# Kernel tuning notes

Hardware: AMD Instinct MI355X
Metric: run time of the kernel (lower is better)

## Reference

```python
import jax, jax.numpy as jnp
import numpy as np

NS, NV = 48, 10            # scalar / vector multiplicities
IN_SIZE = NS + 3*NV + 3*NV + NS   # 156
N_EDGE_FEAT = 96
HIDDEN = 96
# weight shapes per output irrep: 0e:(58,48) 1o:(68,10) 1e:(68,10) 0o:(58,48)
W_SHAPES = [('0e', NS + NV, NS), ('1o', NS + 2*NV, NV), ('1e', 2*NV + NS, NV), ('0o', NV + NS, NS)]
WEIGHT_NUMEL = sum(a*b for _, a, b in W_SHAPES)  # 6928
N_NODES, N_EDGES = 10000, 50000


def setup_inputs() -> dict:
    key = jax.random.key(0)
    ks = jax.random.split(key, 9)
    node_attr = jax.random.normal(ks[0], (N_NODES, IN_SIZE), dtype=jnp.float32)
    edge_index = jax.random.randint(ks[1], (2, N_EDGES), 0, N_NODES)
    edge_attr = jax.random.normal(ks[2], (N_EDGES, N_EDGE_FEAT), dtype=jnp.float32)
    edge_sh = jax.random.normal(ks[3], (N_EDGES, 4), dtype=jnp.float32)
    s1 = 1.0 / np.sqrt(N_EDGE_FEAT)
    s2 = 1.0 / np.sqrt(HIDDEN)
    W1 = jax.random.normal(ks[4], (N_EDGE_FEAT, HIDDEN), dtype=jnp.float32) * s1
    b1 = jnp.zeros((HIDDEN,), dtype=jnp.float32)
    W2 = jax.random.normal(ks[5], (HIDDEN, WEIGHT_NUMEL), dtype=jnp.float32) * s2
    b2 = jnp.zeros((WEIGHT_NUMEL,), dtype=jnp.float32)
    return {'node_attr': node_attr, 'edge_index': edge_index, 'edge_attr': edge_attr,
            'edge_sh': edge_sh, 'W1': W1, 'b1': b1, 'W2': W2, 'b2': b2}


def _faster_tp(in_, sh, weight):
    # in_: [E, 156], sh: [E, 4], weight: [E, 6928]
    in_0e = in_[:, :NS]                                   # [E,48]
    in_1o = in_[:, NS:NS + 3*NV].reshape(-1, NV, 3)       # [E,10,3]
    in_1e = in_[:, NS + 3*NV:NS + 6*NV].reshape(-1, NV, 3)
    in_0o = in_[:, NS + 6*NV:]                            # [E,48]
    sh_0e = sh[:, 0]                                      # [E]
    sh_1o = sh[:, 1:]                                     # [E,3]
    inv_s3 = 1.0 / np.sqrt(3.0)
    inv_s2 = 1.0 / np.sqrt(2.0)

    out_0e = jnp.concatenate([
        in_0e * sh_0e[:, None],
        jnp.sum(in_1o * sh_1o[:, None, :], axis=-1) * inv_s3], axis=-1)      # [E,58]
    out_1o = jnp.concatenate([
        in_0e[:, :, None] * sh_1o[:, None, :],
        in_1o * sh_0e[:, None, None],
        jnp.cross(in_1e, sh_1o[:, None, :]) * inv_s2], axis=-2)              # [E,68,3]
    out_1e = jnp.concatenate([
        jnp.cross(in_1o, sh_1o[:, None, :]) * inv_s2,
        in_1e * sh_0e[:, None, None],
        in_0o[:, :, None] * sh_1o[:, None, :]], axis=-2)                     # [E,68,3]
    out_0o = jnp.concatenate([
        jnp.sum(in_1e * sh_1o[:, None, :], axis=-1) * inv_s3,
        in_0o * sh_0e[:, None]], axis=-1)                                    # [E,58]

    wd = {}
    start = 0
    for name, a, b in W_SHAPES:
        wd[name] = weight[:, start:start + a*b].reshape(-1, a, b) / np.sqrt(a)
        start += a*b

    o0e = jnp.einsum('ei,eio->eo', out_0e, wd['0e'])                 # [E,48]
    o1o = jnp.einsum('eic,eio->eoc', out_1o, wd['1o']).reshape(-1, 3*NV)
    o1e = jnp.einsum('eic,eio->eoc', out_1e, wd['1e']).reshape(-1, 3*NV)
    o0o = jnp.einsum('ei,eio->eo', out_0o, wd['0o'])                 # [E,48]
    return jnp.concatenate([o0e, o1o, o1e, o0o], axis=-1)           # [E,156]


def reference(node_attr, edge_index, edge_attr, edge_sh, W1, b1, W2, b2):
    edge_src, edge_dst = edge_index[0], edge_index[1]
    # edge MLP -> per-edge TP weights
    h = jax.nn.relu(edge_attr @ W1 + b1)
    w = h @ W2 + b2                                       # [E, 6928]
    tp = _faster_tp(node_attr[edge_dst], edge_sh, w)      # [E, 156]
    # scatter-mean over source nodes
    n = node_attr.shape[0]
    seg = jax.ops.segment_sum(tp, edge_src, num_segments=n)
    cnt = jax.ops.segment_sum(jnp.ones((tp.shape[0],), tp.dtype), edge_src, num_segments=n)
    out = seg / jnp.maximum(cnt, 1.0)[:, None]
    # residual (in/out sizes equal, so pad is a no-op)
    return out + node_attr
```

## Files before the change

### kernel.cpp

```cpp
#include <hip/hip_runtime.h>

#define NE 50000
#define NN 10000
#define KH 96
#define WN 6928
#define NTILE 484
#define IN_SZ 156
#define EPW 32

typedef __attribute__((ext_vector_type(8))) short short8;
typedef __attribute__((ext_vector_type(4))) float float4v;

__device__ __forceinline__ unsigned short f2bf(float x) {
  unsigned u = __float_as_uint(x);
  unsigned r = (u + 0x7FFFu + ((u >> 16) & 1u)) >> 16;
  return (unsigned short)r;
}
__device__ __forceinline__ float b2f(unsigned short u) {
  return __uint_as_float(((unsigned)u) << 16);
}

__device__ __forceinline__ void issue3(short8 (&B)[3], float &bv,
                                       const unsigned short* p, const float* pb) {
  asm volatile("global_load_dwordx4 %0, %4, off\n\t"
               "global_load_dwordx4 %1, %4, off offset:1024\n\t"
               "global_load_dwordx4 %2, %4, off offset:2048\n\t"
               "global_load_dword %3, %5, off"
               : "=&v"(B[0]), "=&v"(B[1]), "=&v"(B[2]), "=&v"(bv)
               : "v"(p), "v"(pb));
}
__device__ __forceinline__ void waitB8(short8 (&B)[3], float &bv) {
  asm volatile("s_waitcnt vmcnt(8)"
               : "+v"(B[0]), "+v"(B[1]), "+v"(B[2]), "+v"(bv));
}
__device__ __forceinline__ void waitB4(short8 (&B)[3], float &bv) {
  asm volatile("s_waitcnt vmcnt(4)"
               : "+v"(B[0]), "+v"(B[1]), "+v"(B[2]), "+v"(bv));
}
__device__ __forceinline__ void waitB0(short8 (&B)[3], float &bv) {
  asm volatile("s_waitcnt vmcnt(0)"
               : "+v"(B[0]), "+v"(B[1]), "+v"(B[2]), "+v"(bv));
}

__device__ __forceinline__ int col_of_np(int np) {
  if (np < 2784) return np;
  if (np < 3872) { int rel = np - 2784, i = rel >> 4, o = rel & 15; return (o < 10) ? 2784 + i * 10 + o : -1; }
  if (np < 4960) { int rel = np - 3872, i = rel >> 4, o = rel & 15; return (o < 10) ? 3464 + i * 10 + o : -1; }
  return 4144 + (np - 4960);
}

__global__ __launch_bounds__(256) void w1t_kernel(
    const float* __restrict__ W1, unsigned short* __restrict__ W1T)
{
  int j = blockIdx.x * 256 + threadIdx.x;
  if (j < KH * KH) {
    int c = j / KH, k = j - c * KH;
    W1T[c * KH + k] = f2bf(W1[k * KH + c]);
  }
}

__global__ __launch_bounds__(384) void mlp1_kernel(
    const float* __restrict__ edge_attr, const unsigned short* __restrict__ W1T,
    const float* __restrict__ b1, unsigned short* __restrict__ h_ext)
{
  const int tid = threadIdx.x;
  const int e0 = blockIdx.x * 16;
  const int w = tid >> 6, l = tid & 15, q = (tid >> 4) & 3;

  short8 a[3], b[3];
  #pragma unroll
  for (int s = 0; s < 3; ++s) {
    const float* pa = edge_attr + (size_t)(e0 + l) * KH + s * 32 + q * 8;
    float4 x = *(const float4*)pa, y = *(const float4*)(pa + 4);
    short8 t;
    t[0] = (short)f2bf(x.x); t[1] = (short)f2bf(x.y);
    t[2] = (short)f2bf(x.z); t[3] = (short)f2bf(x.w);
    t[4] = (short)f2bf(y.x); t[5] = (short)f2bf(y.y);
    t[6] = (short)f2bf(y.z); t[7] = (short)f2bf(y.w);
    a[s] = t;
    b[s] = *(const short8*)(W1T + (size_t)(w * 16 + l) * KH + s * 32 + q * 8);
  }
  float4v C = {0.f, 0.f, 0.f, 0.f};
  #pragma unroll
  for (int s = 0; s < 3; ++s)
    C = __builtin_amdgcn_mfma_f32_16x16x32_bf16(a[s], b[s], C, 0, 0, 0);

  float bv = b1[w * 16 + l];
  #pragma unroll
  for (int r = 0; r < 4; ++r)
    h_ext[(size_t)(e0 + q * 4 + r) * KH + w * 16 + l] = f2bf(fmaxf(C[r] + bv, 0.f));
}

__global__ __launch_bounds__(256) void w2pt_kernel(
    const float* __restrict__ W2, const float* __restrict__ b2,
    unsigned short* __restrict__ W2PT, float* __restrict__ b2PT)
{
  int gid = blockIdx.x * 256 + threadIdx.x;
  if (gid < NTILE * 192) {
    int lane = gid & 63, s = (gid >> 6) % 3, t = gid / 192;
    int l = lane & 15, q = lane >> 4;
    int c = col_of_np(t * 16 + l);
    int kbase = s * 32 + q * 8;
    unsigned short o8[8];
    #pragma unroll
    for (int j = 0; j < 8; ++j) {
      int k = kbase + j;
      float v = (c >= 0) ? W2[(size_t)k * WN + c] : 0.f;
      o8[j] = f2bf(v);
    }
    uint4 pk;
    pk.x = o8[0] | ((unsigned)o8[1] << 16);
    pk.y = o8[2] | ((unsigned)o8[3] << 16);
    pk.z = o8[4] | ((unsigned)o8[5] << 16);
    pk.w = o8[6] | ((unsigned)o8[7] << 16);
    *(uint4*)(W2PT + (size_t)gid * 8) = pk;
  } else {
    int j = gid - NTILE * 192;
    if (j < NTILE * 16) {
      int c = col_of_np(j);
      b2PT[j] = (c >= 0) ? b2[c] : 0.f;
    }
  }
}

__global__ __launch_bounds__(512, 4) void tp_kernel(
    const unsigned short* __restrict__ h_ext, const float* __restrict__ node_attr,
    const int* __restrict__ edge_index, const float* __restrict__ edge_sh,
    const unsigned short* __restrict__ W2PT, const float* __restrict__ b2PT,
    float* __restrict__ acc, int* __restrict__ icnt)
{
  __shared__ unsigned short sIn[EPW][160];
  __shared__ float sOut[EPW][IN_SZ];
  __shared__ unsigned short sF0[2][60][EPW];
  __shared__ unsigned short sF1[2][68][3][EPW];
  __shared__ float sShs[EPW][4];
  __shared__ int sSrc[EPW], sDst[EPW];

  const int tid = threadIdx.x;
  const int e0 = blockIdx.x * EPW;

  if (tid < EPW) {
    int ok = (e0 + tid) < NE;
    int s = ok ? edge_index[e0 + tid] : 0;
    int d = ok ? edge_index[NE + e0 + tid] : 0;
    sSrc[tid] = s; sDst[tid] = d;
    if (ok) atomicAdd(&icnt[s], 1);
  }
  if (tid >= 128 && tid < 256) {
    int t2 = tid - 128;
    int e = t2 >> 2, c = t2 & 3;
    sShs[e][c] = ((e0 + e) < NE) ? edge_sh[(size_t)(e0 + e) * 4 + c] : 0.f;
  }
  __syncthreads();

  for (int idx = tid; idx < EPW * IN_SZ; idx += 512) {
    int e = idx / IN_SZ, f = idx - e * IN_SZ;
    sIn[e][f] = f2bf(node_attr[(size_t)sDst[e] * IN_SZ + f]);
  }
  for (int idx = tid; idx < EPW * IN_SZ; idx += 512) (&sOut[0][0])[idx] = 0.f;
  __syncthreads();

  {
    const int e = tid >> 4, j = tid & 15;
    const float sh0 = sShs[e][0], sx = sShs[e][1], sy = sShs[e][2], sz = sShs[e][3];
    const float i3 = 0.57735026918962576f, i2 = 0.70710678118654752f;
    for (int i = j; i < 48; i += 16) {
      float v0 = b2f(sIn[e][i]), w0 = b2f(sIn[e][108 + i]);
      sF0[0][i][e] = f2bf(v0 * sh0);
      sF0[1][10 + i][e] = f2bf(w0 * sh0);
      sF1[0][i][0][e] = f2bf(v0 * sx); sF1[0][i][1][e] = f2bf(v0 * sy); sF1[0][i][2][e] = f2bf(v0 * sz);
      sF1[1][20 + i][0][e] = f2bf(w0 * sx); sF1[1][20 + i][1][e] = f2bf(w0 * sy); sF1[1][20 + i][2][e] = f2bf(w0 * sz);
    }
    if (j < 10) {
      const int v = j;
      float ax = b2f(sIn[e][48 + 3 * v]), ay = b2f(sIn[e][48 + 3 * v + 1]), az = b2f(sIn[e][48 + 3 * v + 2]);
      float bx = b2f(sIn[e][78 + 3 * v]), by = b2f(sIn[e][78 + 3 * v + 1]), bz = b2f(sIn[e][78 + 3 * v + 2]);
      sF0[0][48 + v][e] = f2bf((ax * sx + ay * sy + az * sz) * i3);
      sF0[1][v][e]      = f2bf((bx * sx + by * sy + bz * sz) * i3);
      sF1[0][48 + v][0][e] = f2bf(ax * sh0); sF1[0][48 + v][1][e] = f2bf(ay * sh0); sF1[0][48 + v][2][e] = f2bf(az * sh0);
      sF1[0][58 + v][0][e] = f2bf((by * sz - bz * sy) * i2);
      sF1[0][58 + v][1][e] = f2bf((bz * sx - bx * sz) * i2);
      sF1[0][58 + v][2][e] = f2bf((bx * sy - by * sx) * i2);
      sF1[1][v][0][e] = f2bf((ay * sz - az * sy) * i2);
      sF1[1][v][1][e] = f2bf((az * sx - ax * sz) * i2);
      sF1[1][v][2][e] = f2bf((ax * sy - ay * sx) * i2);
      sF1[1][10 + v][0][e] = f2bf(bx * sh0); sF1[1][10 + v][1][e] = f2bf(by * sh0); sF1[1][10 + v][2][e] = f2bf(bz * sh0);
    }
  }
  if (tid < 128) {
    int fam = tid >> 6, i = 58 + ((tid >> 5) & 1), e = tid & 31;
    sF0[fam][i][e] = 0;
  }
  __syncthreads();

  const int wv = tid >> 6, l = tid & 15, q = (tid >> 4) & 3;

  short8 Af[2][3];
  #pragma unroll
  for (int m = 0; m < 2; ++m) {
    const unsigned short* ar = h_ext + (size_t)(e0 + m * 16 + l) * KH + q * 8;
    #pragma unroll
    for (int s = 0; s < 3; ++s) Af[m][s] = *(const short8*)(ar + s * 32);
  }

  const unsigned short* wlane = W2PT + (size_t)(tid & 63) * 8;
  const float* blane = b2PT + l;

  if (wv < 4) {
    const int sf = wv >> 1;
    const int ibeg = (wv & 1) * 30;
    const int tb = sf ? 310 : 0;
    const int obase = sf ? 108 : 0;
    #pragma unroll 1
    for (int ob = 0; ob < 3; ++ob) {
      float a0[4] = {0.f, 0.f, 0.f, 0.f}, a1[4] = {0.f, 0.f, 0.f, 0.f};
      short8 Ba[3], Bb[3], Bc[3];
      float vA, vB, vC;
      auto taddr = [&](int ii) -> size_t {
        int i = ibeg + ii; if (i >= 58) i = ibeg;
        return (size_t)(tb + 3 * i + ob);
      };
      auto body = [&](const short8 (&B)[3], float bv, int ii) {
        int i = ibeg + ii;
        ushort4 f0 = *(const ushort4*)&sF0[sf][i][q * 4];
        ushort4 f1 = *(const ushort4*)&sF0[sf][i][16 + q * 4];
        float4v C0 = {bv, bv, bv, bv}, C1 = {bv, bv, bv, bv};
        #pragma unroll
        for (int s = 0; s < 3; ++s) {
          C0 = __builtin_amdgcn_mfma_f32_16x16x32_bf16(Af[0][s], B[s], C0, 0, 0, 0);
          C1 = __builtin_amdgcn_mfma_f32_16x16x32_bf16(Af[1][s], B[s], C1, 0, 0, 0);
        }
        a0[0] += C0[0] * b2f(f0.x); a0[1] += C0[1] * b2f(f0.y);
        a0[2] += C0[2] * b2f(f0.z); a0[3] += C0[3] * b2f(f0.w);
        a1[0] += C1[0] * b2f(f1.x); a1[1] += C1[1] * b2f(f1.y);
        a1[2] += C1[2] * b2f(f1.z); a1[3] += C1[3] * b2f(f1.w);
      };
      { size_t t = taddr(0); issue3(Ba, vA, wlane + t * 1536, blane + t * 16); }
      { size_t t = taddr(1); issue3(Bb, vB, wlane + t * 1536, blane + t * 16); }
      { size_t t = taddr(2); issue3(Bc, vC, wlane + t * 1536, blane + t * 16); }
      #pragma unroll 1
      for (int ii = 0; ii < 27; ii += 3) {
        waitB8(Ba, vA); body(Ba, vA, ii);
        { size_t t = taddr(ii + 3); issue3(Ba, vA, wlane + t * 1536, blane + t * 16); }
        waitB8(Bb, vB); body(Bb, vB, ii + 1);
        { size_t t = taddr(ii + 4); issue3(Bb, vB, wlane + t * 1536, blane + t * 16); }
        waitB8(Bc, vC); body(Bc, vC, ii + 2);
        { size_t t = taddr(ii + 5); issue3(Bc, vC, wlane + t * 1536, blane + t * 16); }
      }
      waitB8(Ba, vA); body(Ba, vA, 27);
      waitB4(Bb, vB); body(Bb, vB, 28);
      waitB0(Bc, vC); body(Bc, vC, 29);
      const int col = obase + ob * 16 + l;
      #pragma unroll
      for (int r = 0; r < 4; ++r) {
        unsafeAtomicAdd(&sOut[q * 4 + r][col], a0[r]);
        unsafeAtomicAdd(&sOut[16 + q * 4 + r][col], a1[r]);
      }
    }
  } else {
    const int vf = (wv >> 1) - 2;
    const int ibeg = (wv & 1) * 34;
    const int tb = vf ? 242 : 174;
    float r0[4][3] = {{0.f}}, r1[4][3] = {{0.f}};
    short8 Ba[3], Bb[3];
    float vA, vB;
    auto tadr = [&](int ii) -> size_t { return (size_t)(tb + ibeg + ii); };
    auto body = [&](const short8 (&B)[3], float bv, int ii) {
      int i = ibeg + ii;
      ushort4 g0[3], g1[3];
      #pragma unroll
      for (int cc = 0; cc < 3; ++cc) {
        g0[cc] = *(const ushort4*)&sF1[vf][i][cc][q * 4];
        g1[cc] = *(const ushort4*)&sF1[vf][i][cc][16 + q * 4];
      }
      float4v C0 = {bv, bv, bv, bv}, C1 = {bv, bv, bv, bv};
      #pragma unroll
      for (int s = 0; s < 3; ++s) {
        C0 = __builtin_amdgcn_mfma_f32_16x16x32_bf16(Af[0][s], B[s], C0, 0, 0, 0);
        C1 = __builtin_amdgcn_mfma_f32_16x16x32_bf16(Af[1][s], B[s], C1, 0, 0, 0);
      }
      #pragma unroll
      for (int cc = 0; cc < 3; ++cc) {
        r0[0][cc] += C0[0] * b2f(g0[cc].x); r0[1][cc] += C0[1] * b2f(g0[cc].y);
        r0[2][cc] += C0[2] * b2f(g0[cc].z); r0[3][cc] += C0[3] * b2f(g0[cc].w);
        r1[0][cc] += C1[0] * b2f(g1[cc].x); r1[1][cc] += C1[1] * b2f(g1[cc].y);
        r1[2][cc] += C1[2] * b2f(g1[cc].z); r1[3][cc] += C1[3] * b2f(g1[cc].w);
      }
    };
    { size_t t = tadr(0); issue3(Ba, vA, wlane + t * 1536, blane + t * 16); }
    { size_t t = tadr(1); issue3(Bb, vB, wlane + t * 1536, blane + t * 16); }
    #pragma unroll 1
    for (int ii = 0; ii < 32; ii += 2) {
      waitB4(Ba, vA); body(Ba, vA, ii);
      { size_t t = tadr(ii + 2); issue3(Ba, vA, wlane + t * 1536, blane + t * 16); }
      waitB4(Bb, vB); body(Bb, vB, ii + 1);
      { size_t t = tadr(ii + 3); issue3(Bb, vB, wlane + t * 1536, blane + t * 16); }
    }
    waitB4(Ba, vA); body(Ba, vA, 32);
    waitB0(Bb, vB); body(Bb, vB, 33);
    if (l < 10) {
      const int col = (vf ? 78 : 48) + 3 * l;
      #pragma unroll
      for (int r = 0; r < 4; ++r)
        #pragma unroll
        for (int cc = 0; cc < 3; ++cc) {
          unsafeAtomicAdd(&sOut[q * 4 + r][col + cc], r0[r][cc]);
          unsafeAtomicAdd(&sOut[16 + q * 4 + r][col + cc], r1[r][cc]);
        }
    }
  }
  __syncthreads();

  const float n58 = 0.13130643285972254f, n68 = 0.12126781251816650f;
  for (int idx = tid; idx < EPW * IN_SZ; idx += 512) {
    int e = idx / IN_SZ, o = idx - e * IN_SZ;
    if (e0 + e < NE) {
      float nrm = (o < 48 || o >= 108) ? n58 : n68;
      unsafeAtomicAdd(&acc[(size_t)sSrc[e] * IN_SZ + o], sOut[e][o] * nrm);
    }
  }
}

__global__ __launch_bounds__(256) void finalize_kernel(
    const float* __restrict__ acc, const int* __restrict__ icnt,
    const float* __restrict__ node_attr, float* __restrict__ out)
{
  int idx = blockIdx.x * 256 + threadIdx.x;
  if (idx < NN * IN_SZ) {
    int n = idx / IN_SZ;
    out[idx] = acc[idx] / fmaxf((float)icnt[n], 1.f) + node_attr[idx];
  }
}

extern "C" void kernel_launch(void* const* d_in, const int* in_sizes, int n_in,
                              void* d_out, int out_size, void* d_ws, size_t ws_size,
                              hipStream_t stream)
{
  const float* node_attr  = (const float*)d_in[0];
  const int*   edge_index = (const int*)d_in[1];
  const float* edge_attr  = (const float*)d_in[2];
  const float* edge_sh    = (const float*)d_in[3];
  const float* W1 = (const float*)d_in[4];
  const float* b1 = (const float*)d_in[5];
  const float* W2 = (const float*)d_in[6];
  const float* b2 = (const float*)d_in[7];
  float* out = (float*)d_out;

  unsigned short* h_ext = (unsigned short*)d_ws;
  unsigned short* W2PT  = h_ext + (size_t)50016 * KH;
  float* b2PT = (float*)(W2PT + (size_t)NTILE * 1536);
  float* acc  = b2PT + (size_t)NTILE * 16;
  int*   icnt = (int*)(acc + (size_t)NN * IN_SZ);
  unsigned short* W1T = (unsigned short*)(icnt + NN);

  w1t_kernel<<<(KH * KH + 255) / 256, 256, 0, stream>>>(W1, W1T);
  w2pt_kernel<<<(NTILE * 208 + 255) / 256, 256, 0, stream>>>(W2, b2, W2PT, b2PT);
  mlp1_kernel<<<NE / 16, 384, 0, stream>>>(edge_attr, W1T, b1, h_ext);
  hipMemsetAsync(acc, 0, (size_t)NN * IN_SZ * sizeof(float), stream);
  hipMemsetAsync(icnt, 0, (size_t)NN * sizeof(int), stream);
  hipMemsetAsync(h_ext + (size_t)NE * KH, 0, (size_t)16 * KH * sizeof(unsigned short), stream);
  tp_kernel<<<(NE + EPW - 1) / EPW, 512, 0, stream>>>(h_ext, node_attr, edge_index,
                                                      edge_sh, W2PT, b2PT, acc, icnt);
  finalize_kernel<<<(NN * IN_SZ + 255) / 256, 256, 0, stream>>>(acc, icnt, node_attr, out);
}
```

Measured before the change: 312.3 us.

## Merge prep kernels and memsets, read node_attr directly, rebalance scalar work across waves

Folds the W1 transpose, the W2 pack and the three memsets into one prep kernel, cutting launch and memset overhead. In the TP kernel, the bf16 staging of gathered node_attr in shared memory is dropped; features are built straight from global loads, which removes a barrier and shared-memory traffic. The scalar-irrep input rows are split so the vector waves also take 8 rows each, evening out work across the 8 waves. The shrunken sF0 and uneven padding paths add some risk, and the direct global reads are uncoalesced per lane.

```diff
diff --git a/kernel.cpp b/kernel.cpp
--- a/kernel.cpp
+++ b/kernel.cpp
@@ -10,6 +10,8 @@
 
 typedef __attribute__((ext_vector_type(8))) short short8;
 typedef __attribute__((ext_vector_type(4))) float float4v;
+
+template<int N> struct IC { static constexpr int n = N; };
 
 __device__ __forceinline__ unsigned short f2bf(float x) {
   unsigned u = __float_as_uint(x);
@@ -49,13 +51,56 @@
   return 4144 + (np - 4960);
 }
 
-__global__ __launch_bounds__(256) void w1t_kernel(
-    const float* __restrict__ W1, unsigned short* __restrict__ W1T)
-{
-  int j = blockIdx.x * 256 + threadIdx.x;
-  if (j < KH * KH) {
+#define R0 (NTILE * 192)
+#define R1 (R0 + NTILE * 16)
+#define R2 (R1 + KH * KH)
+#define R3 (R2 + NN * IN_SZ / 4)
+#define R4 (R3 + NN / 4)
+#define R5 (R4 + 192)
+__global__ __launch_bounds__(256) void prep_kernel(
+    const float* __restrict__ W2, const float* __restrict__ b2,
+    const float* __restrict__ W1,
+    unsigned short* __restrict__ W2PT, float* __restrict__ b2PT,
+    unsigned short* __restrict__ W1T,
+    float* __restrict__ acc, int* __restrict__ icnt,
+    unsigned short* __restrict__ h_ext)
+{
+  int gid = blockIdx.x * 256 + threadIdx.x;
+  if (gid < R0) {
+    int lane = gid & 63, s = (gid >> 6) % 3, t = gid / 192;
+    int l = lane & 15, q = lane >> 4;
+    int c = col_of_np(t * 16 + l);
+    int kbase = s * 32 + q * 8;
+    unsigned short o8[8];
+    #pragma unroll
+    for (int j = 0; j < 8; ++j) {
+      int k = kbase + j;
+      float v = (c >= 0) ? W2[(size_t)k * WN + c] : 0.f;
+      o8[j] = f2bf(v);
+    }
+    uint4 pk;
+    pk.x = o8[0] | ((unsigned)o8[1] << 16);
+    pk.y = o8[2] | ((unsigned)o8[3] << 16);
+    pk.z = o8[4] | ((unsigned)o8[5] << 16);
+    pk.w = o8[6] | ((unsigned)o8[7] << 16);
+    *(uint4*)(W2PT + (size_t)gid * 8) = pk;
+  } else if (gid < R1) {
+    int j = gid - R0;
+    int c = col_of_np(j);
+    b2PT[j] = (c >= 0) ? b2[c] : 0.f;
+  } else if (gid < R2) {
+    int j = gid - R1;
     int c = j / KH, k = j - c * KH;
     W1T[c * KH + k] = f2bf(W1[k * KH + c]);
+  } else if (gid < R3) {
+    uint4 z = {0, 0, 0, 0};
+    ((uint4*)acc)[gid - R2] = z;
+  } else if (gid < R4) {
+    uint4 z = {0, 0, 0, 0};
+    ((uint4*)icnt)[gid - R3] = z;
+  } else if (gid < R5) {
+    uint4 z = {0, 0, 0, 0};
+    ((uint4*)(h_ext + (size_t)NE * KH))[gid - R4] = z;
   }
 }
 
@@ -91,47 +136,14 @@
     h_ext[(size_t)(e0 + q * 4 + r) * KH + w * 16 + l] = f2bf(fmaxf(C[r] + bv, 0.f));
 }
 
-__global__ __launch_bounds__(256) void w2pt_kernel(
-    const float* __restrict__ W2, const float* __restrict__ b2,
-    unsigned short* __restrict__ W2PT, float* __restrict__ b2PT)
-{
-  int gid = blockIdx.x * 256 + threadIdx.x;
-  if (gid < NTILE * 192) {
-    int lane = gid & 63, s = (gid >> 6) % 3, t = gid / 192;
-    int l = lane & 15, q = lane >> 4;
-    int c = col_of_np(t * 16 + l);
-    int kbase = s * 32 + q * 8;
-    unsigned short o8[8];
-    #pragma unroll
-    for (int j = 0; j < 8; ++j) {
-      int k = kbase + j;
-      float v = (c >= 0) ? W2[(size_t)k * WN + c] : 0.f;
-      o8[j] = f2bf(v);
-    }
-    uint4 pk;
-    pk.x = o8[0] | ((unsigned)o8[1] << 16);
-    pk.y = o8[2] | ((unsigned)o8[3] << 16);
-    pk.z = o8[4] | ((unsigned)o8[5] << 16);
-    pk.w = o8[6] | ((unsigned)o8[7] << 16);
-    *(uint4*)(W2PT + (size_t)gid * 8) = pk;
-  } else {
-    int j = gid - NTILE * 192;
-    if (j < NTILE * 16) {
-      int c = col_of_np(j);
-      b2PT[j] = (c >= 0) ? b2[c] : 0.f;
-    }
-  }
-}
-
 __global__ __launch_bounds__(512, 4) void tp_kernel(
     const unsigned short* __restrict__ h_ext, const float* __restrict__ node_attr,
     const int* __restrict__ edge_index, const float* __restrict__ edge_sh,
     const unsigned short* __restrict__ W2PT, const float* __restrict__ b2PT,
     float* __restrict__ acc, int* __restrict__ icnt)
 {
-  __shared__ unsigned short sIn[EPW][160];
   __shared__ float sOut[EPW][IN_SZ];
-  __shared__ unsigned short sF0[2][60][EPW];
+  __shared__ unsigned short sF0[2][58][EPW];
   __shared__ unsigned short sF1[2][68][3][EPW];
   __shared__ float sShs[EPW][4];
   __shared__ int sSrc[EPW], sDst[EPW];
@@ -153,19 +165,13 @@
   }
   __syncthreads();
 
-  for (int idx = tid; idx < EPW * IN_SZ; idx += 512) {
-    int e = idx / IN_SZ, f = idx - e * IN_SZ;
-    sIn[e][f] = f2bf(node_attr[(size_t)sDst[e] * IN_SZ + f]);
-  }
-  for (int idx = tid; idx < EPW * IN_SZ; idx += 512) (&sOut[0][0])[idx] = 0.f;
-  __syncthreads();
-
   {
     const int e = tid >> 4, j = tid & 15;
+    const float* na = node_attr + (size_t)sDst[e] * IN_SZ;
     const float sh0 = sShs[e][0], sx = sShs[e][1], sy = sShs[e][2], sz = sShs[e][3];
     const float i3 = 0.57735026918962576f, i2 = 0.70710678118654752f;
     for (int i = j; i < 48; i += 16) {
-      float v0 = b2f(sIn[e][i]), w0 = b2f(sIn[e][108 + i]);
+      float v0 = na[i], w0 = na[108 + i];
       sF0[0][i][e] = f2bf(v0 * sh0);
       sF0[1][10 + i][e] = f2bf(w0 * sh0);
       sF1[0][i][0][e] = f2bf(v0 * sx); sF1[0][i][1][e] = f2bf(v0 * sy); sF1[0][i][2][e] = f2bf(v0 * sz);
@@ -173,8 +179,8 @@
     }
     if (j < 10) {
       const int v = j;
-      float ax = b2f(sIn[e][48 + 3 * v]), ay = b2f(sIn[e][48 + 3 * v + 1]), az = b2f(sIn[e][48 + 3 * v + 2]);
-      float bx = b2f(sIn[e][78 + 3 * v]), by = b2f(sIn[e][78 + 3 * v + 1]), bz = b2f(sIn[e][78 + 3 * v + 2]);
+      float ax = na[48 + 3 * v], ay = na[48 + 3 * v + 1], az = na[48 + 3 * v + 2];
+      float bx = na[78 + 3 * v], by = na[78 + 3 * v + 1], bz = na[78 + 3 * v + 2];
       sF0[0][48 + v][e] = f2bf((ax * sx + ay * sy + az * sz) * i3);
       sF0[1][v][e]      = f2bf((bx * sx + by * sy + bz * sz) * i3);
       sF1[0][48 + v][0][e] = f2bf(ax * sh0); sF1[0][48 + v][1][e] = f2bf(ay * sh0); sF1[0][48 + v][2][e] = f2bf(az * sh0);
@@ -187,10 +193,7 @@
       sF1[1][10 + v][0][e] = f2bf(bx * sh0); sF1[1][10 + v][1][e] = f2bf(by * sh0); sF1[1][10 + v][2][e] = f2bf(bz * sh0);
     }
   }
-  if (tid < 128) {
-    int fam = tid >> 6, i = 58 + ((tid >> 5) & 1), e = tid & 31;
-    sF0[fam][i][e] = 0;
-  }
+  for (int idx = tid; idx < EPW * IN_SZ; idx += 512) (&sOut[0][0])[idx] = 0.f;
   __syncthreads();
 
   const int wv = tid >> 6, l = tid & 15, q = (tid >> 4) & 3;
@@ -206,57 +209,82 @@
   const unsigned short* wlane = W2PT + (size_t)(tid & 63) * 8;
   const float* blane = b2PT + l;
 
-  if (wv < 4) {
-    const int sf = wv >> 1;
-    const int ibeg = (wv & 1) * 30;
-    const int tb = sf ? 310 : 0;
-    const int obase = sf ? 108 : 0;
+  auto sbody = [&](float (&a0)[4], float (&a1)[4], const short8 (&B)[3], float bv,
+                   int sf, int i) {
+    ushort4 f0 = *(const ushort4*)&sF0[sf][i][q * 4];
+    ushort4 f1 = *(const ushort4*)&sF0[sf][i][16 + q * 4];
+    float4v C0 = {bv, bv, bv, bv}, C1 = {bv, bv, bv, bv};
+    #pragma unroll
+    for (int s2 = 0; s2 < 3; ++s2) {
+      C0 = __builtin_amdgcn_mfma_f32_16x16x32_bf16(Af[0][s2], B[s2], C0, 0, 0, 0);
+      C1 = __builtin_amdgcn_mfma_f32_16x16x32_bf16(Af[1][s2], B[s2], C1, 0, 0, 0);
+    }
+    a0[0] += C0[0] * b2f(f0.x); a0[1] += C0[1] * b2f(f0.y);
+    a0[2] += C0[2] * b2f(f0.z); a0[3] += C0[3] * b2f(f0.w);
+    a1[0] += C1[0] * b2f(f1.x); a1[1] += C1[1] * b2f(f1.y);
+    a1[2] += C1[2] * b2f(f1.z); a1[3] += C1[3] * b2f(f1.w);
+  };
+  auto sflush = [&](float (&a0)[4], float (&a1)[4], int col) {
+    #pragma unroll
+    for (int r = 0; r < 4; ++r) {
+      unsafeAtomicAdd(&sOut[q * 4 + r][col],      a0[r]);
+      unsafeAtomicAdd(&sOut[16 + q * 4 + r][col], a1[r]);
+    }
+  };
+
+  auto run_scalar3 = [&](int sf, int ibeg, int tb, int obase, auto cnt) {
+    constexpr int NSTEP = decltype(cnt)::n;
     #pragma unroll 1
     for (int ob = 0; ob < 3; ++ob) {
       float a0[4] = {0.f, 0.f, 0.f, 0.f}, a1[4] = {0.f, 0.f, 0.f, 0.f};
       short8 Ba[3], Bb[3], Bc[3];
       float vA, vB, vC;
-      auto taddr = [&](int ii) -> size_t {
-        int i = ibeg + ii; if (i >= 58) i = ibeg;
-        return (size_t)(tb + 3 * i + ob);
-      };
-      auto body = [&](const short8 (&B)[3], float bv, int ii) {
-        int i = ibeg + ii;
-        ushort4 f0 = *(const ushort4*)&sF0[sf][i][q * 4];
-        ushort4 f1 = *(const ushort4*)&sF0[sf][i][16 + q * 4];
-        float4v C0 = {bv, bv, bv, bv}, C1 = {bv, bv, bv, bv};
-        #pragma unroll
-        for (int s = 0; s < 3; ++s) {
-          C0 = __builtin_amdgcn_mfma_f32_16x16x32_bf16(Af[0][s], B[s], C0, 0, 0, 0);
-          C1 = __builtin_amdgcn_mfma_f32_16x16x32_bf16(Af[1][s], B[s], C1, 0, 0, 0);
-        }
-        a0[0] += C0[0] * b2f(f0.x); a0[1] += C0[1] * b2f(f0.y);
-        a0[2] += C0[2] * b2f(f0.z); a0[3] += C0[3] * b2f(f0.w);
-        a1[0] += C1[0] * b2f(f1.x); a1[1] += C1[1] * b2f(f1.y);
-        a1[2] += C1[2] * b2f(f1.z); a1[3] += C1[3] * b2f(f1.w);
-      };
-      { size_t t = taddr(0); issue3(Ba, vA, wlane + t * 1536, blane + t * 16); }
-      { size_t t = taddr(1); issue3(Bb, vB, wlane + t * 1536, blane + t * 16); }
-      { size_t t = taddr(2); issue3(Bc, vC, wlane + t * 1536, blane + t * 16); }
+      auto tadr = [&](int ii) -> size_t { return (size_t)(tb + 3 * (ibeg + ii) + ob); };
+      { size_t t = tadr(0); issue3(Ba, vA, wlane + t * 1536, blane + t * 16); }
+      { size_t t = tadr(1); issue3(Bb, vB, wlane + t * 1536, blane + t * 16); }
+      { size_t t = tadr(2); issue3(Bc, vC, wlane + t * 1536, blane + t * 16); }
       #pragma unroll 1
-      for (int ii = 0; ii < 27; ii += 3) {
-        waitB8(Ba, vA); body(Ba, vA, ii);
-        { size_t t = taddr(ii + 3); issue3(Ba, vA, wlane + t * 1536, blane + t * 16); }
-        waitB8(Bb, vB); body(Bb, vB, ii + 1);
-        { size_t t = taddr(ii + 4); issue3(Bb, vB, wlane + t * 1536, blane + t * 16); }
-        waitB8(Bc, vC); body(Bc, vC, ii + 2);
-        { size_t t = taddr(ii + 5); issue3(Bc, vC, wlane + t * 1536, blane + t * 16); }
-      }
-      waitB8(Ba, vA); body(Ba, vA, 27);
-      waitB4(Bb, vB); body(Bb, vB, 28);
-      waitB0(Bc, vC); body(Bc, vC, 29);
-      const int col = obase + ob * 16 + l;
-      #pragma unroll
-      for (int r = 0; r < 4; ++r) {
-        unsafeAtomicAdd(&sOut[q * 4 + r][col], a0[r]);
-        unsafeAtomicAdd(&sOut[16 + q * 4 + r][col], a1[r]);
-      }
-    }
+      for (int ii = 0; ii < NSTEP - 3; ii += 3) {
+        waitB8(Ba, vA); sbody(a0, a1, Ba, vA, sf, ibeg + ii);
+        { size_t t = tadr(ii + 3); issue3(Ba, vA, wlane + t * 1536, blane + t * 16); }
+        waitB8(Bb, vB); sbody(a0, a1, Bb, vB, sf, ibeg + ii + 1);
+        { size_t t = tadr(ii + 4); issue3(Bb, vB, wlane + t * 1536, blane + t * 16); }
+        waitB8(Bc, vC); sbody(a0, a1, Bc, vC, sf, ibeg + ii + 2);
+        { size_t t = tadr(ii + 5); issue3(Bc, vC, wlane + t * 1536, blane + t * 16); }
+      }
+      waitB8(Ba, vA); sbody(a0, a1, Ba, vA, sf, ibeg + NSTEP - 3);
+      waitB4(Bb, vB); sbody(a0, a1, Bb, vB, sf, ibeg + NSTEP - 2);
+      waitB0(Bc, vC); sbody(a0, a1, Bc, vC, sf, ibeg + NSTEP - 1);
+      sflush(a0, a1, obase + ob * 16 + l);
+    }
+  };
+
+  auto run_scalar2 = [&](int sf, int ibeg, int tb, int obase, auto cnt) {
+    constexpr int NSTEP = decltype(cnt)::n;
+    #pragma unroll 1
+    for (int ob = 0; ob < 3; ++ob) {
+      float a0[4] = {0.f, 0.f, 0.f, 0.f}, a1[4] = {0.f, 0.f, 0.f, 0.f};
+      short8 Ba[3], Bb[3];
+      float vA, vB;
+      auto tadr = [&](int ii) -> size_t { return (size_t)(tb + 3 * (ibeg + ii) + ob); };
+      { size_t t = tadr(0); issue3(Ba, vA, wlane + t * 1536, blane + t * 16); }
+      { size_t t = tadr(1); issue3(Bb, vB, wlane + t * 1536, blane + t * 16); }
+      #pragma unroll 1
+      for (int ii = 0; ii < NSTEP - 2; ii += 2) {
+        waitB4(Ba, vA); sbody(a0, a1, Ba, vA, sf, ibeg + ii);
+        { size_t t = tadr(ii + 2); issue3(Ba, vA, wlane + t * 1536, blane + t * 16); }
+        waitB4(Bb, vB); sbody(a0, a1, Bb, vB, sf, ibeg + ii + 1);
+        { size_t t = tadr(ii + 3); issue3(Bb, vB, wlane + t * 1536, blane + t * 16); }
+      }
+      waitB4(Ba, vA); sbody(a0, a1, Ba, vA, sf, ibeg + NSTEP - 2);
+      waitB0(Bb, vB); sbody(a0, a1, Bb, vB, sf, ibeg + NSTEP - 1);
+      sflush(a0, a1, obase + ob * 16 + l);
+    }
+  };
+
+  if (wv < 4) {
+    const int sf = wv >> 1;
+    run_scalar3(sf, (wv & 1) * 21, sf ? 310 : 0, sf ? 108 : 0, IC<21>{});
   } else {
     const int vf = (wv >> 1) - 2;
     const int ibeg = (wv & 1) * 34;
@@ -265,7 +293,7 @@
     short8 Ba[3], Bb[3];
     float vA, vB;
     auto tadr = [&](int ii) -> size_t { return (size_t)(tb + ibeg + ii); };
-    auto body = [&](const short8 (&B)[3], float bv, int ii) {
+    auto vbody = [&](const short8 (&B)[3], float bv, int ii) {
       int i = ibeg + ii;
       ushort4 g0[3], g1[3];
       #pragma unroll
@@ -291,13 +319,13 @@
     { size_t t = tadr(1); issue3(Bb, vB, wlane + t * 1536, blane + t * 16); }
     #pragma unroll 1
     for (int ii = 0; ii < 32; ii += 2) {
-      waitB4(Ba, vA); body(Ba, vA, ii);
+      waitB4(Ba, vA); vbody(Ba, vA, ii);
       { size_t t = tadr(ii + 2); issue3(Ba, vA, wlane + t * 1536, blane + t * 16); }
-      waitB4(Bb, vB); body(Bb, vB, ii + 1);
+      waitB4(Bb, vB); vbody(Bb, vB, ii + 1);
       { size_t t = tadr(ii + 3); issue3(Bb, vB, wlane + t * 1536, blane + t * 16); }
     }
-    waitB4(Ba, vA); body(Ba, vA, 32);
-    waitB0(Bb, vB); body(Bb, vB, 33);
+    waitB4(Ba, vA); vbody(Ba, vA, 32);
+    waitB0(Bb, vB); vbody(Bb, vB, 33);
     if (l < 10) {
       const int col = (vf ? 78 : 48) + 3 * l;
       #pragma unroll
@@ -308,6 +336,7 @@
           unsafeAtomicAdd(&sOut[16 + q * 4 + r][col + cc], r1[r][cc]);
         }
     }
+    run_scalar2(vf, 42 + (wv & 1) * 8, vf ? 310 : 0, vf ? 108 : 0, IC<8>{});
   }
   __syncthreads();
 
@@ -353,12 +382,9 @@
   int*   icnt = (int*)(acc + (size_t)NN * IN_SZ);
   unsigned short* W1T = (unsigned short*)(icnt + NN);
 
-  w1t_kernel<<<(KH * KH + 255) / 256, 256, 0, stream>>>(W1, W1T);
-  w2pt_kernel<<<(NTILE * 208 + 255) / 256, 256, 0, stream>>>(W2, b2, W2PT, b2PT);
+  prep_kernel<<<(R5 + 255) / 256, 256, 0, stream>>>(W2, b2, W1, W2PT, b2PT, W1T,
+                                                    acc, icnt, h_ext);
   mlp1_kernel<<<NE / 16, 384, 0, stream>>>(edge_attr, W1T, b1, h_ext);
-  hipMemsetAsync(acc, 0, (size_t)NN * IN_SZ * sizeof(float), stream);
-  hipMemsetAsync(icnt, 0, (size_t)NN * sizeof(int), stream);
-  hipMemsetAsync(h_ext + (size_t)NE * KH, 0, (size_t)16 * KH * sizeof(unsigned short), stream);
   tp_kernel<<<(NE + EPW - 1) / EPW, 512, 0, stream>>>(h_ext, node_attr, edge_index,
                                                       edge_sh, W2PT, b2PT, acc, icnt);
   finalize_kernel<<<(NN * IN_SZ + 255) / 256, 256, 0, stream>>>(acc, icnt, node_attr, out);
```

New measurement: 329.0 us. 1.05x slower.
